# Kernel optimization log

Measured on AMD Instinct MI355X. Metric: run time of the kernel, lower is better.

Reference implementation:

```python
import jax, jax.numpy as jnp
import numpy as np

NUM_HEADS, H, W, B = 32, 64, 64, 512


def cayley_r(p):
    # p: [C, d, d] raw params -> batched Cayley orthogonal R = (I - A) @ (I + A)^{-1}
    p = p.astype(jnp.float32)
    a = 0.5 * (p - jnp.swapaxes(p, -1, -2))          # skew-symmetric A
    eye = jnp.eye(p.shape[-1], dtype=jnp.float32)
    inv_factor = jnp.linalg.solve(eye + a, jnp.broadcast_to(eye, a.shape))
    return (eye - a) @ inv_factor                    # [C, d, d]


def setup_inputs() -> dict:
    key = jax.random.key(0)
    k1, k2, k3 = jax.random.split(key, 3)
    wkv = jax.random.normal(k1, (B, NUM_HEADS, H, W), dtype=jnp.float32)
    p_left = jax.random.normal(k2, (NUM_HEADS, H, H), dtype=jnp.float32)
    p_right = jax.random.normal(k3, (NUM_HEADS, W, W), dtype=jnp.float32)
    return {"wkv": wkv, "p_left": p_left, "p_right": p_right}


def reference(wkv, p_left, p_right):
    r1 = cayley_r(p_left).astype(wkv.dtype)   # [C, h, h]
    r2 = cayley_r(p_right).astype(wkv.dtype)  # [C, w, w]
    # bilateral rotation: out[b,c] = R1[c] @ wkv[b,c] @ R2[c]
    return jnp.einsum('cik,bckl,clj->bcij', r1, wkv, r2)
```

## Files before the change

### kernel.cpp

```cpp
#include <hip/hip_runtime.h>


#define NHEADS 32
#define TILE_ELEMS 4096

typedef __attribute__((ext_vector_type(8))) short bf16x8;
typedef __attribute__((ext_vector_type(16))) float f32x16;
typedef __attribute__((ext_vector_type(4))) unsigned short us4;

static __device__ __forceinline__ unsigned short f2bf(float f) {
    union { float f; unsigned u; } v; v.f = f;
    unsigned r = v.u + 0x7fffu + ((v.u >> 16) & 1u);
    return (unsigned short)(r >> 16);
}

__global__ __launch_bounds__(256) void cayley_kernel(
    const float* __restrict__ p_left, const float* __restrict__ p_right,
    unsigned short* __restrict__ ws_r1, unsigned short* __restrict__ ws_r2t) {
    __shared__ float M[64][65];
    __shared__ float N[64][65];
    __shared__ float fcol[64];

    const int t = threadIdx.x;
    const int side = blockIdx.x >> 5;
    const int c = blockIdx.x & 31;
    const float* p = (side ? p_right : p_left) + c * TILE_ELEMS;

    for (int i = 0; i < 4; ++i) {
        int f = t + 256 * i;
        int r = f >> 4, c4 = f & 15;
        float4 v = ((const float4*)p)[f];
        N[r][c4 * 4 + 0] = v.x; N[r][c4 * 4 + 1] = v.y;
        N[r][c4 * 4 + 2] = v.z; N[r][c4 * 4 + 3] = v.w;
    }
    __syncthreads();

    const int row = t & 63;
    const int jb  = (t >> 6) * 16;

    float mrow[16];
    for (int jj = 0; jj < 16; ++jj) {
        int j = jb + jj;
        float a = 0.5f * (N[row][j] - N[j][row]);
        mrow[jj] = (row == j ? 1.0f : 0.0f) + a;
    }
    __syncthreads();
    for (int jj = 0; jj < 16; ++jj) {
        int j = jb + jj;
        M[row][j] = mrow[jj];
        N[row][j] = (row == j ? 2.0f : 0.0f) - mrow[jj];
    }
    __syncthreads();

    for (int k = 0; k < 64; ++k) {
        if (t < 64) {
            float piv = M[k][k];
            fcol[t] = (t == k) ? 0.0f : M[t][k] / piv;
        }
        __syncthreads();
        float f = fcol[row];
        if (f != 0.0f) {
            for (int jj = 0; jj < 16; ++jj) {
                int j = jb + jj;
                M[row][j] -= f * M[k][j];
                N[row][j] -= f * N[k][j];
            }
        }
        __syncthreads();
    }

    float dinv = 1.0f / M[row][row];
    if (side == 0) {
        unsigned short* dst = ws_r1 + c * TILE_ELEMS;
        for (int jj = 0; jj < 16; ++jj) {
            int j = jb + jj;
            dst[row * 64 + j] = f2bf(N[row][j] * dinv);
        }
    } else {
        unsigned short* dst = ws_r2t + c * TILE_ELEMS;
        for (int jj = 0; jj < 16; ++jj) {
            int j = jb + jj;
            dst[j * 64 + row] = f2bf(N[row][j] * dinv);
        }
    }
}

__global__ __launch_bounds__(256, 4) void rot_kernel(
    const float* __restrict__ wkv,
    const unsigned short* __restrict__ ws_r1,
    const unsigned short* __restrict__ ws_r2t,
    float* __restrict__ out) {
    __shared__ unsigned short Wl[64][72];
    __shared__ unsigned short R1l[64][72];
    __shared__ unsigned short R2Tl[64][72];
    __shared__ unsigned short UTl[64][72];

    const int t = threadIdx.x;
    const int c = blockIdx.x & 31;
    const float* wtile = wkv + ((size_t)blockIdx.x << 12);

    for (int i = 0; i < 4; ++i) {
        int f = t + 256 * i;
        int r = f >> 4, c4 = f & 15;
        float4 v = ((const float4*)wtile)[f];
        us4 o;
        o[0] = f2bf(v.x); o[1] = f2bf(v.y); o[2] = f2bf(v.z); o[3] = f2bf(v.w);
        *(us4*)&Wl[r][c4 * 4] = o;
    }
    {
        const us4* s1 = (const us4*)(ws_r1 + c * TILE_ELEMS);
        const us4* s2 = (const us4*)(ws_r2t + c * TILE_ELEMS);
        for (int i = 0; i < 4; ++i) {
            int f = t + 256 * i;
            int r = f >> 4, c4 = f & 15;
            *(us4*)&R1l[r][c4 * 4]  = s1[f];
            *(us4*)&R2Tl[r][c4 * 4] = s2[f];
        }
    }
    __syncthreads();

    const int lane = t & 63;
    const int wave = t >> 6;
    const int l31 = lane & 31;
    const int lhi = lane >> 5;
    const int wr = (wave & 1) * 32;
    const int wc = (wave >> 1) * 32;
    const int m = wr + l31;
    const int n = wc + l31;

    f32x16 acc;
#pragma unroll
    for (int i = 0; i < 16; ++i) acc[i] = 0.0f;
#pragma unroll
    for (int kb = 0; kb < 4; ++kb) {
        int k0 = kb * 16 + lhi * 8;
        bf16x8 a = *(const bf16x8*)&Wl[m][k0];
        bf16x8 b = *(const bf16x8*)&R2Tl[n][k0];
        acc = __builtin_amdgcn_mfma_f32_32x32x16_bf16(a, b, acc, 0, 0, 0);
    }
#pragma unroll
    for (int g = 0; g < 4; ++g) {
        int kbase = wr + 8 * g + 4 * lhi;
        us4 v;
#pragma unroll
        for (int q = 0; q < 4; ++q) v[q] = f2bf(acc[4 * g + q]);
        *(us4*)&UTl[n][kbase] = v;
    }
    __syncthreads();

    f32x16 acc2;
#pragma unroll
    for (int i = 0; i < 16; ++i) acc2[i] = 0.0f;
#pragma unroll
    for (int kb = 0; kb < 4; ++kb) {
        int k0 = kb * 16 + lhi * 8;
        bf16x8 a = *(const bf16x8*)&R1l[m][k0];
        bf16x8 b = *(const bf16x8*)&UTl[n][k0];
        acc2 = __builtin_amdgcn_mfma_f32_32x32x16_bf16(a, b, acc2, 0, 0, 0);
    }

    float* otile = out + ((size_t)blockIdx.x << 12);
#pragma unroll
    for (int g = 0; g < 4; ++g) {
#pragma unroll
        for (int q = 0; q < 4; ++q) {
            int rowl = 8 * g + 4 * lhi + q;
            otile[(size_t)(wr + rowl) * 64 + wc + l31] = acc2[4 * g + q];
        }
    }
}

extern "C" void kernel_launch(void* const* d_in, const int* in_sizes, int n_in,
                              void* d_out, int out_size, void* d_ws, size_t ws_size,
                              hipStream_t stream) {
    const float* wkv     = (const float*)d_in[0];
    const float* p_left  = (const float*)d_in[1];
    const float* p_right = (const float*)d_in[2];
    float* out = (float*)d_out;

    unsigned short* ws_r1  = (unsigned short*)d_ws;
    unsigned short* ws_r2t = ws_r1 + NHEADS * TILE_ELEMS;

    cayley_kernel<<<64, 256, 0, stream>>>(p_left, p_right, ws_r1, ws_r2t);

    int ntiles = in_sizes[0] / TILE_ELEMS;
    rot_kernel<<<ntiles, 256, 0, stream>>>(wkv, ws_r1, ws_r2t, out);
}
```

Measured before the change: 485.3 us.

## Register-resident Gauss-Jordan in Cayley kernel; persistent multi-tile rotation with prefetch

The Cayley solve now keeps each thread's M and N row slices in registers. Only the pivot row and column are broadcast through double-buffered shared memory, which cuts the barriers per step from two to one and removes the full-matrix shared-memory updates. The rotation kernel now processes 8 tiles of the same head per block, so R1/R2 are loaded once per block, and it prefetches the next wkv tile into registers while the MFMAs run. The cost is fewer blocks (2048 instead of 16384) and more registers, which may reduce latency hiding; Wl reuse across iterations relies on the second barrier.

```diff
diff --git a/kernel.cpp b/kernel.cpp
--- a/kernel.cpp
+++ b/kernel.cpp
@@ -3,6 +3,7 @@
 
 #define NHEADS 32
 #define TILE_ELEMS 4096
+#define TPB 8
 
 typedef __attribute__((ext_vector_type(8))) short bf16x8;
 typedef __attribute__((ext_vector_type(16))) float f32x16;
@@ -17,9 +18,11 @@
 __global__ __launch_bounds__(256) void cayley_kernel(
     const float* __restrict__ p_left, const float* __restrict__ p_right,
     unsigned short* __restrict__ ws_r1, unsigned short* __restrict__ ws_r2t) {
-    __shared__ float M[64][65];
-    __shared__ float N[64][65];
-    __shared__ float fcol[64];
+    __shared__ float P[64][68];
+    __shared__ float frowM[2][64];
+    __shared__ float frowN[2][64];
+    __shared__ float fcol[2][64];
+    __shared__ float dinv_l[64];
 
     const int t = threadIdx.x;
     const int side = blockIdx.x >> 5;
@@ -29,59 +32,66 @@
     for (int i = 0; i < 4; ++i) {
         int f = t + 256 * i;
         int r = f >> 4, c4 = f & 15;
-        float4 v = ((const float4*)p)[f];
-        N[r][c4 * 4 + 0] = v.x; N[r][c4 * 4 + 1] = v.y;
-        N[r][c4 * 4 + 2] = v.z; N[r][c4 * 4 + 3] = v.w;
+        *(float4*)&P[r][c4 * 4] = ((const float4*)p)[f];
     }
     __syncthreads();
 
     const int row = t & 63;
-    const int jb  = (t >> 6) * 16;
-
-    float mrow[16];
+    const int sl  = t >> 6;
+    const int jb  = sl * 16;
+
+    float mreg[16], nreg[16];
+#pragma unroll
     for (int jj = 0; jj < 16; ++jj) {
         int j = jb + jj;
-        float a = 0.5f * (N[row][j] - N[j][row]);
-        mrow[jj] = (row == j ? 1.0f : 0.0f) + a;
-    }
+        float a = 0.5f * (P[row][j] - P[j][row]);
+        float e = (row == j) ? 1.0f : 0.0f;
+        mreg[jj] = e + a;
+        nreg[jj] = e - a;
+    }
+
+    int buf = 0;
+    for (int k = 0; k < 64; ++k) {
+        const int kb = k >> 4, kk = k & 15;
+        if (row == k) {
+#pragma unroll
+            for (int jj = 0; jj < 16; ++jj) {
+                frowM[buf][jb + jj] = mreg[jj];
+                frowN[buf][jb + jj] = nreg[jj];
+            }
+        }
+        if (sl == kb) fcol[buf][row] = mreg[kk];
+        __syncthreads();
+        float pinv = __builtin_amdgcn_rcpf(frowM[buf][k]);
+        float f = fcol[buf][row] * pinv;
+        if (row != k) {
+#pragma unroll
+            for (int jj = 0; jj < 16; ++jj) {
+                mreg[jj] -= f * frowM[buf][jb + jj];
+                nreg[jj] -= f * frowN[buf][jb + jj];
+            }
+        }
+        buf ^= 1;
+    }
+
+    if (sl == (row >> 4)) dinv_l[row] = __builtin_amdgcn_rcpf(mreg[row & 15]);
     __syncthreads();
-    for (int jj = 0; jj < 16; ++jj) {
-        int j = jb + jj;
-        M[row][j] = mrow[jj];
-        N[row][j] = (row == j ? 2.0f : 0.0f) - mrow[jj];
-    }
-    __syncthreads();
-
-    for (int k = 0; k < 64; ++k) {
-        if (t < 64) {
-            float piv = M[k][k];
-            fcol[t] = (t == k) ? 0.0f : M[t][k] / piv;
-        }
-        __syncthreads();
-        float f = fcol[row];
-        if (f != 0.0f) {
-            for (int jj = 0; jj < 16; ++jj) {
-                int j = jb + jj;
-                M[row][j] -= f * M[k][j];
-                N[row][j] -= f * N[k][j];
-            }
-        }
-        __syncthreads();
-    }
-
-    float dinv = 1.0f / M[row][row];
+    const float dinv = dinv_l[row];
+
     if (side == 0) {
         unsigned short* dst = ws_r1 + c * TILE_ELEMS;
-        for (int jj = 0; jj < 16; ++jj) {
-            int j = jb + jj;
-            dst[row * 64 + j] = f2bf(N[row][j] * dinv);
+#pragma unroll
+        for (int q4 = 0; q4 < 4; ++q4) {
+            us4 v;
+#pragma unroll
+            for (int q = 0; q < 4; ++q) v[q] = f2bf(nreg[q4 * 4 + q] * dinv);
+            *(us4*)&dst[row * 64 + jb + q4 * 4] = v;
         }
     } else {
         unsigned short* dst = ws_r2t + c * TILE_ELEMS;
-        for (int jj = 0; jj < 16; ++jj) {
-            int j = jb + jj;
-            dst[j * 64 + row] = f2bf(N[row][j] * dinv);
-        }
+#pragma unroll
+        for (int jj = 0; jj < 16; ++jj)
+            dst[(jb + jj) * 64 + row] = f2bf(nreg[jj] * dinv);
     }
 }
 
@@ -90,23 +100,16 @@
     const unsigned short* __restrict__ ws_r1,
     const unsigned short* __restrict__ ws_r2t,
     float* __restrict__ out) {
-    __shared__ unsigned short Wl[64][72];
     __shared__ unsigned short R1l[64][72];
     __shared__ unsigned short R2Tl[64][72];
+    __shared__ unsigned short Wl[64][72];
     __shared__ unsigned short UTl[64][72];
 
     const int t = threadIdx.x;
     const int c = blockIdx.x & 31;
-    const float* wtile = wkv + ((size_t)blockIdx.x << 12);
-
-    for (int i = 0; i < 4; ++i) {
-        int f = t + 256 * i;
-        int r = f >> 4, c4 = f & 15;
-        float4 v = ((const float4*)wtile)[f];
-        us4 o;
-        o[0] = f2bf(v.x); o[1] = f2bf(v.y); o[2] = f2bf(v.z); o[3] = f2bf(v.w);
-        *(us4*)&Wl[r][c4 * 4] = o;
-    }
+    const int bg = blockIdx.x >> 5;
+    const size_t tile0 = (size_t)(bg * TPB) * NHEADS + c;
+
     {
         const us4* s1 = (const us4*)(ws_r1 + c * TILE_ELEMS);
         const us4* s2 = (const us4*)(ws_r2t + c * TILE_ELEMS);
@@ -117,7 +120,13 @@
             *(us4*)&R2Tl[r][c4 * 4] = s2[f];
         }
     }
-    __syncthreads();
+
+    float4 pf[4];
+    {
+        const float4* wt = (const float4*)(wkv + tile0 * TILE_ELEMS);
+#pragma unroll
+        for (int i = 0; i < 4; ++i) pf[i] = wt[t + 256 * i];
+    }
 
     const int lane = t & 63;
     const int wave = t >> 6;
@@ -128,44 +137,63 @@
     const int m = wr + l31;
     const int n = wc + l31;
 
-    f32x16 acc;
-#pragma unroll
-    for (int i = 0; i < 16; ++i) acc[i] = 0.0f;
-#pragma unroll
-    for (int kb = 0; kb < 4; ++kb) {
-        int k0 = kb * 16 + lhi * 8;
-        bf16x8 a = *(const bf16x8*)&Wl[m][k0];
-        bf16x8 b = *(const bf16x8*)&R2Tl[n][k0];
-        acc = __builtin_amdgcn_mfma_f32_32x32x16_bf16(a, b, acc, 0, 0, 0);
-    }
-#pragma unroll
-    for (int g = 0; g < 4; ++g) {
-        int kbase = wr + 8 * g + 4 * lhi;
-        us4 v;
-#pragma unroll
-        for (int q = 0; q < 4; ++q) v[q] = f2bf(acc[4 * g + q]);
-        *(us4*)&UTl[n][kbase] = v;
-    }
-    __syncthreads();
-
-    f32x16 acc2;
-#pragma unroll
-    for (int i = 0; i < 16; ++i) acc2[i] = 0.0f;
-#pragma unroll
-    for (int kb = 0; kb < 4; ++kb) {
-        int k0 = kb * 16 + lhi * 8;
-        bf16x8 a = *(const bf16x8*)&R1l[m][k0];
-        bf16x8 b = *(const bf16x8*)&UTl[n][k0];
-        acc2 = __builtin_amdgcn_mfma_f32_32x32x16_bf16(a, b, acc2, 0, 0, 0);
-    }
-
-    float* otile = out + ((size_t)blockIdx.x << 12);
-#pragma unroll
-    for (int g = 0; g < 4; ++g) {
-#pragma unroll
-        for (int q = 0; q < 4; ++q) {
-            int rowl = 8 * g + 4 * lhi + q;
-            otile[(size_t)(wr + rowl) * 64 + wc + l31] = acc2[4 * g + q];
+    for (int j = 0; j < TPB; ++j) {
+#pragma unroll
+        for (int i = 0; i < 4; ++i) {
+            int f = t + 256 * i;
+            int r = f >> 4, c4 = f & 15;
+            us4 o;
+            o[0] = f2bf(pf[i].x); o[1] = f2bf(pf[i].y);
+            o[2] = f2bf(pf[i].z); o[3] = f2bf(pf[i].w);
+            *(us4*)&Wl[r][c4 * 4] = o;
+        }
+        __syncthreads();
+
+        if (j + 1 < TPB) {
+            const float4* wn = (const float4*)(wkv + (tile0 + (size_t)(j + 1) * NHEADS) * TILE_ELEMS);
+#pragma unroll
+            for (int i = 0; i < 4; ++i) pf[i] = wn[t + 256 * i];
+        }
+
+        f32x16 acc;
+#pragma unroll
+        for (int i = 0; i < 16; ++i) acc[i] = 0.0f;
+#pragma unroll
+        for (int kb = 0; kb < 4; ++kb) {
+            int k0 = kb * 16 + lhi * 8;
+            bf16x8 a = *(const bf16x8*)&Wl[m][k0];
+            bf16x8 b = *(const bf16x8*)&R2Tl[n][k0];
+            acc = __builtin_amdgcn_mfma_f32_32x32x16_bf16(a, b, acc, 0, 0, 0);
+        }
+#pragma unroll
+        for (int g = 0; g < 4; ++g) {
+            int kbase = wr + 8 * g + 4 * lhi;
+            us4 v;
+#pragma unroll
+            for (int q = 0; q < 4; ++q) v[q] = f2bf(acc[4 * g + q]);
+            *(us4*)&UTl[n][kbase] = v;
+        }
+        __syncthreads();
+
+        f32x16 acc2;
+#pragma unroll
+        for (int i = 0; i < 16; ++i) acc2[i] = 0.0f;
+#pragma unroll
+        for (int kb = 0; kb < 4; ++kb) {
+            int k0 = kb * 16 + lhi * 8;
+            bf16x8 a = *(const bf16x8*)&R1l[m][k0];
+            bf16x8 b = *(const bf16x8*)&UTl[n][k0];
+            acc2 = __builtin_amdgcn_mfma_f32_32x32x16_bf16(a, b, acc2, 0, 0, 0);
+        }
+
+        float* otile = out + (tile0 + (size_t)j * NHEADS) * TILE_ELEMS;
+#pragma unroll
+        for (int g = 0; g < 4; ++g) {
+#pragma unroll
+            for (int q = 0; q < 4; ++q) {
+                int rowl = 8 * g + 4 * lhi + q;
+                otile[(size_t)(wr + rowl) * 64 + wc + l31] = acc2[4 * g + q];
+            }
         }
     }
 }
@@ -184,5 +212,5 @@
     cayley_kernel<<<64, 256, 0, stream>>>(p_left, p_right, ws_r1, ws_r2t);
 
     int ntiles = in_sizes[0] / TILE_ELEMS;
-    rot_kernel<<<ntiles, 256, 0, stream>>>(wkv, ws_r1, ws_r2t, out);
-}
+    rot_kernel<<<ntiles / TPB, 256, 0, stream>>>(wkv, ws_r1, ws_r2t, out);
+}
```

After: 477.1 us. About the same (-1.7%).
